# Performance work log

Hardware: AMD Instinct MI355X
Metric: run time of the kernel (lower is better)

The kernel has to match this reference:

```python
import jax, jax.numpy as jnp
import numpy as np

DIM = 512
HEADS = 8
HEAD_DIM = DIM // HEADS
NEG = -1e9


def setup_inputs() -> dict:
    key = jax.random.key(0)
    ks = jax.random.split(key, 12)
    B, S, D = 1, 4096, DIM
    x = jax.random.normal(ks[0], (B, S, D), dtype=jnp.float32)
    coords = jax.random.uniform(ks[1], (B, S, 2), dtype=jnp.float32) * 100.0
    attn_mask = jax.random.randint(ks[2], (B, S, S), 0, 2).astype(bool)
    alibi_mask = jax.random.randint(ks[3], (B, S, S), 0, 2).astype(bool)
    sc = 1.0 / np.sqrt(D)
    params = dict(
        ln_g=jnp.ones((D,), jnp.float32),
        ln_b=jnp.zeros((D,), jnp.float32),
        Wq=jax.random.normal(ks[4], (D, D), jnp.float32) * sc,
        bq=jnp.zeros((D,), jnp.float32),
        Wk=jax.random.normal(ks[5], (D, D), jnp.float32) * sc,
        bk=jnp.zeros((D,), jnp.float32),
        Wv=jax.random.normal(ks[6], (D, D), jnp.float32) * sc,
        bv=jnp.zeros((D,), jnp.float32),
        Wo=jax.random.normal(ks[7], (D, D), jnp.float32) * sc,
        bo=jnp.zeros((D,), jnp.float32),
    )
    return {"x": x, "coords": coords, "attn_mask": attn_mask,
            "alibi_mask": alibi_mask, **params}


def reference(x, coords, attn_mask, alibi_mask,
              ln_g, ln_b, Wq, bq, Wk, bk, Wv, bv, Wo, bo):
    B, S, D = x.shape
    H, d = HEADS, HEAD_DIM
    # LayerNorm
    mu = jnp.mean(x, axis=-1, keepdims=True)
    var = jnp.mean(jnp.square(x - mu), axis=-1, keepdims=True)
    xn = (x - mu) * jax.lax.rsqrt(var + 1e-5) * ln_g + ln_b
    # per-head Q,K,V projections  [B,H,S,d]
    q = (xn @ Wq + bq).reshape(B, S, H, d).transpose(0, 2, 1, 3)
    k = (xn @ Wk + bk).reshape(B, S, H, d).transpose(0, 2, 1, 3)
    v = (xn @ Wv + bv).reshape(B, S, H, d).transpose(0, 2, 1, 3)
    scores = jnp.einsum('bhqd,bhkd->bhqk', q, k) / jnp.sqrt(jnp.float32(d))
    # ALiBi bias from Euclidean distance between tile coordinates, per-head slope
    dist = jnp.sqrt(jnp.sum(jnp.square(coords[:, :, None, :] - coords[:, None, :, :]),
                            axis=-1) + 1e-12)              # [B,S,S]
    slopes = 2.0 ** (-8.0 * jnp.arange(1, H + 1, dtype=jnp.float32) / H)  # [H]
    bias = -slopes[None, :, None, None] * (dist[:, None] * alibi_mask[:, None].astype(jnp.float32))
    scores = scores + bias
    # attn_mask[b,q,k]==True -> query q may NOT attend to key k
    scores = jnp.where(attn_mask[:, None], NEG, scores)
    attn = jax.nn.softmax(scores, axis=-1)                  # [B,H,S,S]
    out = jnp.einsum('bhqk,bhkd->bhqd', attn, v)
    out = out.transpose(0, 2, 1, 3).reshape(B, S, D) @ Wo + bo
    return out, attn
```

## Files before the change

### kernel.cpp

```cpp
#include <hip/hip_runtime.h>
#include <hip/hip_bf16.h>
#include <stdint.h>

#define S 4096
#define D 512
#define H 8
#define HD 64
#define SW 128

typedef __attribute__((ext_vector_type(8))) short bf16x8;
typedef __attribute__((ext_vector_type(4))) float f32x4;

__device__ inline f32x4 mfma16(bf16x8 a, bf16x8 b, f32x4 c) {
  return __builtin_amdgcn_mfma_f32_16x16x32_bf16(a, b, c, 0, 0, 0);
}

__device__ inline unsigned short f2bf(float f) {
  union { __hip_bfloat16 h; unsigned short u; } cv;
  cv.h = __float2bfloat16(f);
  return cv.u;
}
__device__ inline float bf2f(unsigned short u) {
  union { unsigned short u; __hip_bfloat16 h; } cv;
  cv.u = u;
  return __bfloat162float(cv.h);
}

__global__ __launch_bounds__(64) void detect_kernel(
    const unsigned char* __restrict__ a, int* __restrict__ flag) {
  int t = threadIdx.x;
  int v = a[t * 4 + 1] | a[t * 4 + 2] | a[t * 4 + 3];
#pragma unroll
  for (int o = 1; o < 64; o <<= 1) v |= __shfl_xor(v, o);
  if (t == 0) *flag = (v == 0) ? 4 : 1;
}

__global__ __launch_bounds__(256) void compress_kernel(
    const unsigned char* __restrict__ am, const unsigned char* __restrict__ lm,
    const int* __restrict__ mflag, unsigned int* __restrict__ abits,
    unsigned int* __restrict__ lbits) {
  const int row = blockIdx.x;
  const int w = threadIdx.x >> 6, lane = threadIdx.x & 63;
  const size_t ms = (size_t)(*mflag);
#pragma unroll
  for (int it = 0; it < 16; it++) {
    int c0 = w * 1024 + it * 64;
    size_t idx = ((size_t)row * S + c0 + lane) * ms;
    unsigned long long ba = __ballot(am[idx] != 0);
    unsigned long long bl = __ballot(lm[idx] != 0);
    if (lane == 0) {
      int wi = row * SW + (c0 >> 5);
      abits[wi] = (unsigned int)ba;
      abits[wi + 1] = (unsigned int)(ba >> 32);
      lbits[wi] = (unsigned int)bl;
      lbits[wi + 1] = (unsigned int)(bl >> 32);
    }
  }
}

__global__ __launch_bounds__(256) void ln_kernel(
    const float* __restrict__ x, const float* __restrict__ g,
    const float* __restrict__ b, unsigned short* __restrict__ xnh,
    unsigned short* __restrict__ xnl) {
  int row = blockIdx.x;
  int t = threadIdx.x;
  float2 v = reinterpret_cast<const float2*>(x + (size_t)row * D)[t];
  float s = v.x + v.y;
  float s2 = v.x * v.x + v.y * v.y;
#pragma unroll
  for (int o = 1; o < 64; o <<= 1) {
    s += __shfl_xor(s, o);
    s2 += __shfl_xor(s2, o);
  }
  __shared__ float red[8];
  int wid = t >> 6;
  if ((t & 63) == 0) { red[wid] = s; red[4 + wid] = s2; }
  __syncthreads();
  s = red[0] + red[1] + red[2] + red[3];
  s2 = red[4] + red[5] + red[6] + red[7];
  float mu = s * (1.f / D);
  float var = s2 * (1.f / D) - mu * mu;
  float rsig = rsqrtf(var + 1e-5f);
  int i0 = 2 * t, i1 = 2 * t + 1;
  float xn0 = (v.x - mu) * rsig * g[i0] + b[i0];
  float xn1 = (v.y - mu) * rsig * g[i1] + b[i1];
  unsigned short h0 = f2bf(xn0), h1 = f2bf(xn1);
  size_t base = (size_t)row * D;
  xnh[base + i0] = h0;
  xnh[base + i1] = h1;
  xnl[base + i0] = f2bf(xn0 - bf2f(h0));
  xnl[base + i1] = f2bf(xn1 - bf2f(h1));
}

__global__ __launch_bounds__(256) void wsplit_kernel(
    const float* __restrict__ Wq, const float* __restrict__ Wk,
    const float* __restrict__ Wv, const float* __restrict__ Wo,
    unsigned short* __restrict__ qh, unsigned short* __restrict__ ql,
    unsigned short* __restrict__ kh, unsigned short* __restrict__ kl,
    unsigned short* __restrict__ vh, unsigned short* __restrict__ oh) {
  __shared__ float tile[64][65];
  int m = blockIdx.z;
  const float* W = (m == 0) ? Wq : (m == 1) ? Wk : (m == 2) ? Wv : Wo;
  int bx = blockIdx.x * 64;
  int by = blockIdx.y * 64;
  int tx = threadIdx.x & 63, ty = threadIdx.x >> 6;
#pragma unroll
  for (int i = 0; i < 16; i++) {
    int r = ty + i * 4;
    tile[r][tx] = W[(size_t)(by + r) * D + bx + tx];
  }
  __syncthreads();
#pragma unroll
  for (int i = 0; i < 16; i++) {
    int r = ty + i * 4;
    float w = tile[tx][r];
    unsigned short hi = f2bf(w);
    size_t to = (size_t)(bx + r) * D + by + tx;
    if (m == 0) { qh[to] = hi; ql[to] = f2bf(w - bf2f(hi)); }
    else if (m == 1) { kh[to] = hi; kl[to] = f2bf(w - bf2f(hi)); }
    else if (m == 2) { vh[to] = hi; }
    else { oh[to] = hi; }
  }
}

__global__ __launch_bounds__(256) void qkv_kernel(
    const unsigned short* __restrict__ xnh, const unsigned short* __restrict__ xnl,
    const unsigned short* __restrict__ wqh, const unsigned short* __restrict__ wql,
    const unsigned short* __restrict__ wkh, const unsigned short* __restrict__ wkl,
    const unsigned short* __restrict__ wvh,
    const float* __restrict__ bq, const float* __restrict__ bk,
    const float* __restrict__ bv,
    unsigned short* __restrict__ Qb, unsigned short* __restrict__ Kb,
    unsigned short* __restrict__ VT) {
  int z = blockIdx.z;
  int wave = threadIdx.x >> 6, lane = threadIdx.x & 63;
  int lg = lane >> 4, lr = lane & 15;
  int rtile = blockIdx.x * 64 + wave * 16;
  int ctile = blockIdx.y * 64;
  const unsigned short* wh = (z == 0) ? wqh : (z == 1) ? wkh : wvh;
  const unsigned short* wl = (z == 0) ? wql : wkl;
  const float* bias = (z == 0) ? bq : (z == 1) ? bk : bv;
  f32x4 zero = {0.f, 0.f, 0.f, 0.f};
  f32x4 acc[4] = {zero, zero, zero, zero};
  int ar = rtile + lr;
  const unsigned short* ap = xnh + (size_t)ar * D + lg * 8;
  const unsigned short* apl = xnl + (size_t)ar * D + lg * 8;
  for (int kk = 0; kk < D; kk += 32) {
    bf16x8 ah = *(const bf16x8*)(ap + kk);
    bf16x8 al = {};
    if (z < 2) al = *(const bf16x8*)(apl + kk);
#pragma unroll
    for (int nt = 0; nt < 4; nt++) {
      size_t bo_ = (size_t)(ctile + nt * 16 + lr) * D + kk + lg * 8;
      bf16x8 bh = *(const bf16x8*)(wh + bo_);
      acc[nt] = mfma16(ah, bh, acc[nt]);
      if (z < 2) {
        bf16x8 bl = *(const bf16x8*)(wl + bo_);
        acc[nt] = mfma16(ah, bl, acc[nt]);
        acc[nt] = mfma16(al, bh, acc[nt]);
      }
    }
  }
#pragma unroll
  for (int nt = 0; nt < 4; nt++) {
    int col = ctile + nt * 16 + lr;
    float bb = bias[col];
#pragma unroll
    for (int r = 0; r < 4; r++) {
      int row = rtile + lg * 4 + r;
      float val = acc[nt][r] + bb;
      if (z == 0) Qb[(size_t)row * D + col] = f2bf(val);
      else if (z == 1) Kb[(size_t)row * D + col] = f2bf(val);
      else VT[(size_t)col * S + row] = f2bf(val);
    }
  }
}

__global__ __launch_bounds__(512, 4) void attn_kernel(
    const unsigned short* __restrict__ Qb, const unsigned short* __restrict__ Kb,
    const unsigned short* __restrict__ VT,
    const unsigned int* __restrict__ abits,
    const unsigned int* __restrict__ lbits,
    const float* __restrict__ coords,
    float* __restrict__ attn, unsigned short* __restrict__ OH) {
  __shared__ float dm[32][132];
  __shared__ __align__(16) unsigned short pB[8][16][136];
  const int tid = threadIdx.x;
  const int wave = tid >> 6, lane = tid & 63;
  const int bid = blockIdx.x;
  const int xcd = bid & 7, slot = bid >> 3;
  const int qblock = ((xcd & 3) * 32 + slot) * 32;
  const int h = (xcd >> 2) * 4 + (wave & 3);
  const int qoff = (wave >> 2) * 16;
  const int lg = lane >> 4, lr = lane & 15;
  const int qbase = qblock + qoff;
  const float L2E = 1.4426950408889634f;
  const float A2 = 0.125f * L2E;
  const float B2 = exp2f(-(float)(h + 1)) * L2E;
  const float C2 = -50.f * L2E;
  bf16x8 qf0, qf1;
  {
    const unsigned short* qp = Qb + (size_t)(qbase + lr) * D + h * HD + lg * 8;
    qf0 = *(const bf16x8*)qp;
    qf1 = *(const bf16x8*)(qp + 32);
  }
  float lsum[4] = {0.f, 0.f, 0.f, 0.f};

  for (int kt = 0; kt < S; kt += 128) {
    __syncthreads();
#pragma unroll
    for (int p = 0; p < 8; p++) {
      int idx = tid + p * 512;
      int qi = idx >> 7, kj = idx & 127;
      int q = qblock + qi, k = kt + kj;
      int wi = q * SW + ((kt + kj) >> 5);
      float dv = 0.f;
      if ((abits[wi] >> (kj & 31)) & 1u) dv = 1e30f;
      else if ((lbits[wi] >> (kj & 31)) & 1u) {
        float dx = coords[2 * q] - coords[2 * k];
        float dy = coords[2 * q + 1] - coords[2 * k + 1];
        dv = sqrtf(dx * dx + dy * dy + 1e-12f);
      }
      dm[qi][kj] = dv;
    }
    __syncthreads();
#pragma unroll
    for (int kk = 0; kk < 8; kk++) {
      const unsigned short* kp = Kb + (size_t)(kt + kk * 16 + lr) * D + h * HD + lg * 8;
      bf16x8 kf0 = *(const bf16x8*)kp;
      bf16x8 kf1 = *(const bf16x8*)(kp + 32);
      f32x4 c = {0.f, 0.f, 0.f, 0.f};
      c = mfma16(qf0, kf0, c);
      c = mfma16(qf1, kf1, c);
#pragma unroll
      for (int r = 0; r < 4; r++) {
        float t = fmaf(c[r], A2, fmaf(-B2, dm[qoff + lg * 4 + r][kk * 16 + lr], C2));
        lsum[r] += exp2f(t);
      }
    }
  }
#pragma unroll
  for (int r = 0; r < 4; r++) {
#pragma unroll
    for (int o = 1; o < 16; o <<= 1) lsum[r] += __shfl_xor(lsum[r], o);
  }
  float rl[4];
#pragma unroll
  for (int r = 0; r < 4; r++) rl[r] = 1.f / lsum[r];
  f32x4 zero = {0.f, 0.f, 0.f, 0.f};
  f32x4 oacc[4] = {zero, zero, zero, zero};

  for (int kt = 0; kt < S; kt += 128) {
    __syncthreads();
#pragma unroll
    for (int p = 0; p < 8; p++) {
      int idx = tid + p * 512;
      int qi = idx >> 7, kj = idx & 127;
      int q = qblock + qi, k = kt + kj;
      int wi = q * SW + ((kt + kj) >> 5);
      float dv = 0.f;
      if ((abits[wi] >> (kj & 31)) & 1u) dv = 1e30f;
      else if ((lbits[wi] >> (kj & 31)) & 1u) {
        float dx = coords[2 * q] - coords[2 * k];
        float dy = coords[2 * q + 1] - coords[2 * k + 1];
        dv = sqrtf(dx * dx + dy * dy + 1e-12f);
      }
      dm[qi][kj] = dv;
    }
    __syncthreads();
#pragma unroll
    for (int kk = 0; kk < 8; kk++) {
      const unsigned short* kp = Kb + (size_t)(kt + kk * 16 + lr) * D + h * HD + lg * 8;
      bf16x8 kf0 = *(const bf16x8*)kp;
      bf16x8 kf1 = *(const bf16x8*)(kp + 32);
      f32x4 c = {0.f, 0.f, 0.f, 0.f};
      c = mfma16(qf0, kf0, c);
      c = mfma16(qf1, kf1, c);
#pragma unroll
      for (int r = 0; r < 4; r++) {
        float t = fmaf(c[r], A2, fmaf(-B2, dm[qoff + lg * 4 + r][kk * 16 + lr], C2));
        float pv = exp2f(t) * rl[r];
        __builtin_nontemporal_store(
            pv, &attn[((size_t)h * S + qbase + lg * 4 + r) * S + kt + kk * 16 + lr]);
        pB[wave][lg * 4 + r][kk * 16 + lr] = f2bf(pv);
      }
    }
#pragma unroll
    for (int ks = 0; ks < 4; ks++) {
      bf16x8 pa = *(const bf16x8*)&pB[wave][lr][ks * 32 + lg * 8];
#pragma unroll
      for (int nt = 0; nt < 4; nt++) {
        const unsigned short* vp =
            VT + (size_t)(h * HD + nt * 16 + lr) * S + kt + ks * 32 + lg * 8;
        bf16x8 vb = *(const bf16x8*)vp;
        oacc[nt] = mfma16(pa, vb, oacc[nt]);
      }
    }
  }
#pragma unroll
  for (int nt = 0; nt < 4; nt++) {
#pragma unroll
    for (int r = 0; r < 4; r++) {
      OH[(size_t)(qbase + lg * 4 + r) * D + h * HD + nt * 16 + lr] =
          f2bf(oacc[nt][r]);
    }
  }
}

__global__ __launch_bounds__(256) void oproj_kernel(
    const unsigned short* __restrict__ OH, const unsigned short* __restrict__ woh,
    const float* __restrict__ bo, float* __restrict__ out) {
  int wave = threadIdx.x >> 6, lane = threadIdx.x & 63;
  int lg = lane >> 4, lr = lane & 15;
  int rtile = blockIdx.x * 64 + wave * 16;
  int ctile = blockIdx.y * 64;
  f32x4 zero = {0.f, 0.f, 0.f, 0.f};
  f32x4 acc[4] = {zero, zero, zero, zero};
  const unsigned short* ap = OH + (size_t)(rtile + lr) * D + lg * 8;
  for (int kk = 0; kk < D; kk += 32) {
    bf16x8 a = *(const bf16x8*)(ap + kk);
#pragma unroll
    for (int nt = 0; nt < 4; nt++) {
      bf16x8 b = *(const bf16x8*)(woh + (size_t)(ctile + nt * 16 + lr) * D + kk + lg * 8);
      acc[nt] = mfma16(a, b, acc[nt]);
    }
  }
#pragma unroll
  for (int nt = 0; nt < 4; nt++) {
    int col = ctile + nt * 16 + lr;
    float bb = bo[col];
#pragma unroll
    for (int r = 0; r < 4; r++) {
      out[(size_t)(rtile + lg * 4 + r) * D + col] = acc[nt][r] + bb;
    }
  }
}

extern "C" void kernel_launch(void* const* d_in, const int* in_sizes, int n_in,
                              void* d_out, int out_size, void* d_ws,
                              size_t ws_size, hipStream_t stream) {
  const float* x = (const float*)d_in[0];
  const float* coords = (const float*)d_in[1];
  const unsigned char* amask = (const unsigned char*)d_in[2];
  const unsigned char* almask = (const unsigned char*)d_in[3];
  const float* ln_g = (const float*)d_in[4];
  const float* ln_b = (const float*)d_in[5];
  const float* Wq = (const float*)d_in[6];
  const float* bq = (const float*)d_in[7];
  const float* Wk = (const float*)d_in[8];
  const float* bk = (const float*)d_in[9];
  const float* Wv = (const float*)d_in[10];
  const float* bv = (const float*)d_in[11];
  const float* Wo = (const float*)d_in[12];
  const float* bo = (const float*)d_in[13];

  float* out = (float*)d_out;
  float* attn = out + (size_t)S * D;

  char* w = (char*)d_ws;
  int* mflag = (int*)w; w += 256;
  const size_t sz_xn = (size_t)S * D * 2;
  const size_t sz_w = (size_t)D * D * 2;
  const size_t sz_bits = (size_t)S * SW * 4;
  unsigned short* xnh = (unsigned short*)w; w += sz_xn;
  unsigned short* xnl = (unsigned short*)w; w += sz_xn;
  unsigned short* wqh = (unsigned short*)w; w += sz_w;
  unsigned short* wql = (unsigned short*)w; w += sz_w;
  unsigned short* wkh = (unsigned short*)w; w += sz_w;
  unsigned short* wkl = (unsigned short*)w; w += sz_w;
  unsigned short* wvh = (unsigned short*)w; w += sz_w;
  unsigned short* woh = (unsigned short*)w; w += sz_w;
  unsigned short* Qb = (unsigned short*)w; w += sz_xn;
  unsigned short* Kb = (unsigned short*)w; w += sz_xn;
  unsigned short* VT = (unsigned short*)w; w += sz_xn;
  unsigned short* OH = (unsigned short*)w; w += sz_xn;
  unsigned int* abits = (unsigned int*)w; w += sz_bits;
  unsigned int* lbits = (unsigned int*)w; w += sz_bits;

  detect_kernel<<<1, 64, 0, stream>>>(amask, mflag);
  compress_kernel<<<S, 256, 0, stream>>>(amask, almask, mflag, abits, lbits);
  ln_kernel<<<S, 256, 0, stream>>>(x, ln_g, ln_b, xnh, xnl);
  wsplit_kernel<<<dim3(8, 8, 4), 256, 0, stream>>>(Wq, Wk, Wv, Wo, wqh, wql,
                                                   wkh, wkl, wvh, woh);
  qkv_kernel<<<dim3(64, 8, 3), 256, 0, stream>>>(xnh, xnl, wqh, wql, wkh, wkl,
                                                 wvh, bq, bk, bv, Qb, Kb, VT);
  attn_kernel<<<256, 512, 0, stream>>>(Qb, Kb, VT, abits, lbits,
                                       coords, attn, OH);
  oproj_kernel<<<dim3(64, 8), 256, 0, stream>>>(OH, woh, bo, out);
}
```

Before: 1.315 ms.

## Split attention into key-chunked sum and write kernels and vectorize mask compression

Splits the single attention kernel into two launches. The first computes partial softmax denominators over four key chunks. The second reads those partials and writes probabilities and partial outputs over two key chunks. This raises the grid from 256 blocks to 1024 and 512 blocks, with every head of a 16-query tile in one block, so there is more parallelism and the mask and distance tile is shared across heads. The output projection now sums the two fp32 partial outputs before converting to bf16, which adds extra workspace traffic. Mask compression is rewritten to use vectorized per-thread loads and bit packing instead of ballots.

```diff
diff --git a/kernel.cpp b/kernel.cpp
--- a/kernel.cpp
+++ b/kernel.cpp
@@ -7,6 +7,8 @@
 #define H 8
 #define HD 64
 #define SW 128
+#define KC_SUM 4
+#define KC_WR 2
 
 typedef __attribute__((ext_vector_type(8))) short bf16x8;
 typedef __attribute__((ext_vector_type(4))) float f32x4;
@@ -35,27 +37,40 @@
   if (t == 0) *flag = (v == 0) ? 4 : 1;
 }
 
-__global__ __launch_bounds__(256) void compress_kernel(
+__global__ __launch_bounds__(128) void compress_kernel(
     const unsigned char* __restrict__ am, const unsigned char* __restrict__ lm,
     const int* __restrict__ mflag, unsigned int* __restrict__ abits,
     unsigned int* __restrict__ lbits) {
   const int row = blockIdx.x;
-  const int w = threadIdx.x >> 6, lane = threadIdx.x & 63;
-  const size_t ms = (size_t)(*mflag);
-#pragma unroll
-  for (int it = 0; it < 16; it++) {
-    int c0 = w * 1024 + it * 64;
-    size_t idx = ((size_t)row * S + c0 + lane) * ms;
-    unsigned long long ba = __ballot(am[idx] != 0);
-    unsigned long long bl = __ballot(lm[idx] != 0);
-    if (lane == 0) {
-      int wi = row * SW + (c0 >> 5);
-      abits[wi] = (unsigned int)ba;
-      abits[wi + 1] = (unsigned int)(ba >> 32);
-      lbits[wi] = (unsigned int)bl;
-      lbits[wi + 1] = (unsigned int)(bl >> 32);
-    }
-  }
+  const int t = threadIdx.x;
+  const int ms = *mflag;
+  unsigned int wa = 0, wl = 0;
+  const size_t gi = (size_t)row * (S / 4) + t * 8;
+  if (ms == 1) {
+    const uchar4* pa = reinterpret_cast<const uchar4*>(am) + gi;
+    const uchar4* pl = reinterpret_cast<const uchar4*>(lm) + gi;
+#pragma unroll
+    for (int j = 0; j < 8; j++) {
+      uchar4 va = pa[j], vl = pl[j];
+      wa |= (unsigned)(va.x != 0) << (j * 4) | (unsigned)(va.y != 0) << (j * 4 + 1) |
+            (unsigned)(va.z != 0) << (j * 4 + 2) | (unsigned)(va.w != 0) << (j * 4 + 3);
+      wl |= (unsigned)(vl.x != 0) << (j * 4) | (unsigned)(vl.y != 0) << (j * 4 + 1) |
+            (unsigned)(vl.z != 0) << (j * 4 + 2) | (unsigned)(vl.w != 0) << (j * 4 + 3);
+    }
+  } else {
+    const int4* pa = reinterpret_cast<const int4*>(am) + gi;
+    const int4* pl = reinterpret_cast<const int4*>(lm) + gi;
+#pragma unroll
+    for (int j = 0; j < 8; j++) {
+      int4 va = pa[j], vl = pl[j];
+      wa |= (unsigned)(va.x != 0) << (j * 4) | (unsigned)(va.y != 0) << (j * 4 + 1) |
+            (unsigned)(va.z != 0) << (j * 4 + 2) | (unsigned)(va.w != 0) << (j * 4 + 3);
+      wl |= (unsigned)(vl.x != 0) << (j * 4) | (unsigned)(vl.y != 0) << (j * 4 + 1) |
+            (unsigned)(vl.z != 0) << (j * 4 + 2) | (unsigned)(vl.w != 0) << (j * 4 + 3);
+    }
+  }
+  abits[row * SW + t] = wa;
+  lbits[row * SW + t] = wl;
 }
 
 __global__ __launch_bounds__(256) void ln_kernel(
@@ -176,24 +191,17 @@
   }
 }
 
-__global__ __launch_bounds__(512, 4) void attn_kernel(
+__global__ __launch_bounds__(512, 8) void attn_sum_kernel(
     const unsigned short* __restrict__ Qb, const unsigned short* __restrict__ Kb,
-    const unsigned short* __restrict__ VT,
-    const unsigned int* __restrict__ abits,
-    const unsigned int* __restrict__ lbits,
-    const float* __restrict__ coords,
-    float* __restrict__ attn, unsigned short* __restrict__ OH) {
-  __shared__ float dm[32][132];
-  __shared__ __align__(16) unsigned short pB[8][16][136];
+    const unsigned int* __restrict__ abits, const unsigned int* __restrict__ lbits,
+    const float* __restrict__ coords, float* __restrict__ Lpart) {
+  __shared__ float dm[16][132];
   const int tid = threadIdx.x;
   const int wave = tid >> 6, lane = tid & 63;
-  const int bid = blockIdx.x;
-  const int xcd = bid & 7, slot = bid >> 3;
-  const int qblock = ((xcd & 3) * 32 + slot) * 32;
-  const int h = (xcd >> 2) * 4 + (wave & 3);
-  const int qoff = (wave >> 2) * 16;
+  const int h = wave;
   const int lg = lane >> 4, lr = lane & 15;
-  const int qbase = qblock + qoff;
+  const int qbase = blockIdx.x * 16;
+  const int kc = blockIdx.y;
   const float L2E = 1.4426950408889634f;
   const float A2 = 0.125f * L2E;
   const float B2 = exp2f(-(float)(h + 1)) * L2E;
@@ -205,15 +213,15 @@
     qf1 = *(const bf16x8*)(qp + 32);
   }
   float lsum[4] = {0.f, 0.f, 0.f, 0.f};
-
-  for (int kt = 0; kt < S; kt += 128) {
+  const int kt0 = kc * (S / KC_SUM);
+  for (int kt = kt0; kt < kt0 + S / KC_SUM; kt += 128) {
     __syncthreads();
 #pragma unroll
-    for (int p = 0; p < 8; p++) {
+    for (int p = 0; p < 4; p++) {
       int idx = tid + p * 512;
       int qi = idx >> 7, kj = idx & 127;
-      int q = qblock + qi, k = kt + kj;
-      int wi = q * SW + ((kt + kj) >> 5);
+      int q = qbase + qi, k = kt + kj;
+      int wi = q * SW + (k >> 5);
       float dv = 0.f;
       if ((abits[wi] >> (kj & 31)) & 1u) dv = 1e30f;
       else if ((lbits[wi] >> (kj & 31)) & 1u) {
@@ -234,7 +242,7 @@
       c = mfma16(qf1, kf1, c);
 #pragma unroll
       for (int r = 0; r < 4; r++) {
-        float t = fmaf(c[r], A2, fmaf(-B2, dm[qoff + lg * 4 + r][kk * 16 + lr], C2));
+        float t = fmaf(c[r], A2, fmaf(-B2, dm[lg * 4 + r][kk * 16 + lr], C2));
         lsum[r] += exp2f(t);
       }
     }
@@ -244,20 +252,58 @@
 #pragma unroll
     for (int o = 1; o < 16; o <<= 1) lsum[r] += __shfl_xor(lsum[r], o);
   }
+  if (lr == 0) {
+#pragma unroll
+    for (int r = 0; r < 4; r++) {
+      Lpart[((size_t)kc * H + h) * S + qbase + lg * 4 + r] = lsum[r];
+    }
+  }
+}
+
+__global__ __launch_bounds__(512, 4) void attn_write_kernel(
+    const unsigned short* __restrict__ Qb, const unsigned short* __restrict__ Kb,
+    const unsigned short* __restrict__ VT,
+    const unsigned int* __restrict__ abits, const unsigned int* __restrict__ lbits,
+    const float* __restrict__ coords, const float* __restrict__ Lpart,
+    float* __restrict__ attn, float* __restrict__ OHp) {
+  __shared__ float dm[16][132];
+  __shared__ __align__(16) unsigned short pB[8][16][136];
+  const int tid = threadIdx.x;
+  const int wave = tid >> 6, lane = tid & 63;
+  const int h = wave;
+  const int lg = lane >> 4, lr = lane & 15;
+  const int qbase = blockIdx.x * 16;
+  const int kc = blockIdx.y;
+  const float L2E = 1.4426950408889634f;
+  const float A2 = 0.125f * L2E;
+  const float B2 = exp2f(-(float)(h + 1)) * L2E;
+  const float C2 = -50.f * L2E;
+  bf16x8 qf0, qf1;
+  {
+    const unsigned short* qp = Qb + (size_t)(qbase + lr) * D + h * HD + lg * 8;
+    qf0 = *(const bf16x8*)qp;
+    qf1 = *(const bf16x8*)(qp + 32);
+  }
   float rl[4];
 #pragma unroll
-  for (int r = 0; r < 4; r++) rl[r] = 1.f / lsum[r];
+  for (int r = 0; r < 4; r++) {
+    int row = qbase + lg * 4 + r;
+    float ls = 0.f;
+#pragma unroll
+    for (int c = 0; c < KC_SUM; c++) ls += Lpart[((size_t)c * H + h) * S + row];
+    rl[r] = 1.f / ls;
+  }
   f32x4 zero = {0.f, 0.f, 0.f, 0.f};
   f32x4 oacc[4] = {zero, zero, zero, zero};
-
-  for (int kt = 0; kt < S; kt += 128) {
+  const int kt0 = kc * (S / KC_WR);
+  for (int kt = kt0; kt < kt0 + S / KC_WR; kt += 128) {
     __syncthreads();
 #pragma unroll
-    for (int p = 0; p < 8; p++) {
+    for (int p = 0; p < 4; p++) {
       int idx = tid + p * 512;
       int qi = idx >> 7, kj = idx & 127;
-      int q = qblock + qi, k = kt + kj;
-      int wi = q * SW + ((kt + kj) >> 5);
+      int q = qbase + qi, k = kt + kj;
+      int wi = q * SW + (k >> 5);
       float dv = 0.f;
       if ((abits[wi] >> (kj & 31)) & 1u) dv = 1e30f;
       else if ((lbits[wi] >> (kj & 31)) & 1u) {
@@ -278,7 +324,7 @@
       c = mfma16(qf1, kf1, c);
 #pragma unroll
       for (int r = 0; r < 4; r++) {
-        float t = fmaf(c[r], A2, fmaf(-B2, dm[qoff + lg * 4 + r][kk * 16 + lr], C2));
+        float t = fmaf(c[r], A2, fmaf(-B2, dm[lg * 4 + r][kk * 16 + lr], C2));
         float pv = exp2f(t) * rl[r];
         __builtin_nontemporal_store(
             pv, &attn[((size_t)h * S + qbase + lg * 4 + r) * S + kt + kk * 16 + lr]);
@@ -301,14 +347,14 @@
   for (int nt = 0; nt < 4; nt++) {
 #pragma unroll
     for (int r = 0; r < 4; r++) {
-      OH[(size_t)(qbase + lg * 4 + r) * D + h * HD + nt * 16 + lr] =
-          f2bf(oacc[nt][r]);
+      OHp[((size_t)kc * S + qbase + lg * 4 + r) * D + h * HD + nt * 16 + lr] =
+          oacc[nt][r];
     }
   }
 }
 
 __global__ __launch_bounds__(256) void oproj_kernel(
-    const unsigned short* __restrict__ OH, const unsigned short* __restrict__ woh,
+    const float* __restrict__ OHp, const unsigned short* __restrict__ woh,
     const float* __restrict__ bo, float* __restrict__ out) {
   int wave = threadIdx.x >> 6, lane = threadIdx.x & 63;
   int lg = lane >> 4, lr = lane & 15;
@@ -316,13 +362,23 @@
   int ctile = blockIdx.y * 64;
   f32x4 zero = {0.f, 0.f, 0.f, 0.f};
   f32x4 acc[4] = {zero, zero, zero, zero};
-  const unsigned short* ap = OH + (size_t)(rtile + lr) * D + lg * 8;
+  const float* p0 = OHp + (size_t)(rtile + lr) * D;
+  const float* p1 = OHp + ((size_t)S + rtile + lr) * D;
   for (int kk = 0; kk < D; kk += 32) {
-    bf16x8 a = *(const bf16x8*)(ap + kk);
+    int base = kk + lg * 8;
+    float4 a0 = *(const float4*)(p0 + base);
+    float4 a1 = *(const float4*)(p0 + base + 4);
+    float4 b0 = *(const float4*)(p1 + base);
+    float4 b1 = *(const float4*)(p1 + base + 4);
+    union { unsigned short u[8]; bf16x8 v; } A;
+    A.u[0] = f2bf(a0.x + b0.x); A.u[1] = f2bf(a0.y + b0.y);
+    A.u[2] = f2bf(a0.z + b0.z); A.u[3] = f2bf(a0.w + b0.w);
+    A.u[4] = f2bf(a1.x + b1.x); A.u[5] = f2bf(a1.y + b1.y);
+    A.u[6] = f2bf(a1.z + b1.z); A.u[7] = f2bf(a1.w + b1.w);
 #pragma unroll
     for (int nt = 0; nt < 4; nt++) {
       bf16x8 b = *(const bf16x8*)(woh + (size_t)(ctile + nt * 16 + lr) * D + kk + lg * 8);
-      acc[nt] = mfma16(a, b, acc[nt]);
+      acc[nt] = mfma16(A.v, b, acc[nt]);
     }
   }
 #pragma unroll
@@ -373,18 +429,21 @@
   unsigned short* Qb = (unsigned short*)w; w += sz_xn;
   unsigned short* Kb = (unsigned short*)w; w += sz_xn;
   unsigned short* VT = (unsigned short*)w; w += sz_xn;
-  unsigned short* OH = (unsigned short*)w; w += sz_xn;
   unsigned int* abits = (unsigned int*)w; w += sz_bits;
   unsigned int* lbits = (unsigned int*)w; w += sz_bits;
+  float* Lpart = (float*)w; w += (size_t)KC_SUM * H * S * 4;
+  float* OHp = (float*)w; w += (size_t)KC_WR * S * D * 4;
 
   detect_kernel<<<1, 64, 0, stream>>>(amask, mflag);
-  compress_kernel<<<S, 256, 0, stream>>>(amask, almask, mflag, abits, lbits);
+  compress_kernel<<<S, 128, 0, stream>>>(amask, almask, mflag, abits, lbits);
   ln_kernel<<<S, 256, 0, stream>>>(x, ln_g, ln_b, xnh, xnl);
   wsplit_kernel<<<dim3(8, 8, 4), 256, 0, stream>>>(Wq, Wk, Wv, Wo, wqh, wql,
                                                    wkh, wkl, wvh, woh);
   qkv_kernel<<<dim3(64, 8, 3), 256, 0, stream>>>(xnh, xnl, wqh, wql, wkh, wkl,
                                                  wvh, bq, bk, bv, Qb, Kb, VT);
-  attn_kernel<<<256, 512, 0, stream>>>(Qb, Kb, VT, abits, lbits,
-                                       coords, attn, OH);
-  oproj_kernel<<<dim3(64, 8), 256, 0, stream>>>(OH, woh, bo, out);
-}
+  attn_sum_kernel<<<dim3(S / 16, KC_SUM), 512, 0, stream>>>(
+      Qb, Kb, abits, lbits, coords, Lpart);
+  attn_write_kernel<<<dim3(S / 16, KC_WR), 512, 0, stream>>>(
+      Qb, Kb, VT, abits, lbits, coords, Lpart, attn, OHp);
+  oproj_kernel<<<dim3(64, 8), 256, 0, stream>>>(OHp, woh, bo, out);
+}
```

New measurement: 1.240 ms. 1.06x faster.
